# Optimization experiments

Hardware: AMD Instinct MI355X
Metric: run time of the kernel (lower is better)

Reference implementation:

```python
import jax, jax.numpy as jnp
import numpy as np
from jax import lax

L = 500
THRESH_INIT = 1.7
THRESH_STEP = 0.1
NUM_ADJ_PARM = 0.3


def _maxpool2(x):
    # 2x2 max pool, stride 2, NCHW
    return lax.reduce_window(x, -jnp.inf, lax.max, (1, 1, 2, 2), (1, 1, 2, 2), 'VALID')


def setup_inputs() -> dict:
    key = jax.random.key(0)
    ks = jax.random.split(key, 10)
    N = 2048
    s = 0.05
    return {
        'x': jax.random.normal(ks[0], (1, N, 1, 28, 28), dtype=jnp.float32),
        'conv1_w': jax.random.normal(ks[1], (20, 1, 5, 5), dtype=jnp.float32) * s,
        'conv1_b': jnp.zeros((20,), dtype=jnp.float32),
        'conv2_w': jax.random.normal(ks[2], (50, 20, 5, 5), dtype=jnp.float32) * s,
        'conv2_b': jnp.zeros((50,), dtype=jnp.float32),
        'fc_w': jax.random.normal(ks[3], (800, L), dtype=jnp.float32) * s,
        'fc_b': jnp.zeros((L,), dtype=jnp.float32),
        'gcn_w': jax.random.normal(ks[4], (L, L), dtype=jnp.float32) * s,
        'gcn_b': jnp.zeros((L,), dtype=jnp.float32),
    }


def reference(x, conv1_w, conv1_b, conv2_w, conv2_b, fc_w, fc_b, gcn_w, gcn_b):
    dn = ('NCHW', 'OIHW', 'NCHW')
    h = x[0]  # squeeze(0) -> [N,1,28,28]
    h = lax.conv_general_dilated(h, conv1_w, (1, 1), 'VALID', dimension_numbers=dn)
    h = _maxpool2(jax.nn.relu(h + conv1_b[None, :, None, None]))  # [N,20,12,12]
    h = lax.conv_general_dilated(h, conv2_w, (1, 1), 'VALID', dimension_numbers=dn)
    h = _maxpool2(jax.nn.relu(h + conv2_b[None, :, None, None]))  # [N,50,4,4]
    h = h.reshape(-1, 50 * 4 * 4)  # [N,800]
    H = jax.nn.relu(h @ fc_w + fc_b)  # [N,L]

    n_nodes = H.shape[0]
    sq = jnp.sum(H * H, axis=1)
    d2 = sq[:, None] + sq[None, :] - 2.0 * (H @ H.T)
    dist = jnp.sqrt(jnp.maximum(d2, 0.0))  # [N,N]

    eye = jnp.eye(n_nodes, dtype=bool)
    dist_sg = lax.stop_gradient(dist)
    min_edges = NUM_ADJ_PARM * n_nodes

    def cond(thr):
        cnt = jnp.sum(((dist_sg < thr) & ~eye).astype(jnp.float32))
        return cnt < min_edges

    thr = lax.while_loop(cond, lambda t: t + jnp.float32(THRESH_STEP),
                         jnp.float32(THRESH_INIT))

    adj = ((dist_sg < thr) & ~eye).astype(H.dtype)
    a_hat = adj + jnp.eye(n_nodes, dtype=H.dtype)
    dinv = lax.rsqrt(jnp.sum(a_hat, axis=1))  # deg >= 1 (self-loops)
    norm_adj = a_hat * dinv[:, None] * dinv[None, :]
    out = norm_adj @ (H @ gcn_w) + gcn_b  # [N,L]
    return jax.nn.log_softmax(out, axis=-1)
```

## Files before the change

### kernel.cpp

```cpp
#include <hip/hip_runtime.h>
#include <math.h>


#define NN 2048
#define LL 500
#define NBIN 512

#define KEEP(x) asm volatile("" : "+v"(x))

#define O_POOL1 ((size_t)0)
#define O_POOL2 (O_POOL1 + (size_t)2048*2880)
#define O_H     (O_POOL2 + (size_t)2048*800)
#define O_HW    (O_H     + (size_t)2048*500)
#define O_DIST  (O_HW    + (size_t)2048*500)
#define O_SQ    (O_DIST  + (size_t)2048*2048)
#define O_TBL   (O_SQ    + 2048)
#define O_HIST  (O_TBL   + NBIN)
#define O_THR   (O_HIST  + NBIN)
#define O_DINV  (O_THR   + 16)

__device__ __forceinline__ float4 ldg4_tail(const float* p, int rem) {
    float4 v;
    if (rem >= 4) v = *(const float4*)p;
    else {
        v.x = (rem > 0) ? p[0] : 0.f;
        v.y = (rem > 1) ? p[1] : 0.f;
        v.z = (rem > 2) ? p[2] : 0.f;
        v.w = (rem > 3) ? p[3] : 0.f;
    }
    return v;
}

__device__ __forceinline__ float4 zero4() { float4 v; v.x = v.y = v.z = v.w = 0.f; return v; }

__global__ void k_init(float* __restrict__ tbl, unsigned* __restrict__ hist) {
    int t = threadIdx.x;
    if (t == 0) {
        float v = 1.7f;
        for (int k = 0; k < NBIN; k++) { tbl[k] = v; v += 0.1f; }
    }
    for (int i = t; i < NBIN; i += 256) hist[i] = 0u;
}

__global__ __launch_bounds__(512)
void k_conv1(const float* __restrict__ x, const float* __restrict__ w,
             const float* __restrict__ b, float* __restrict__ out) {
    __shared__ float xin[4 * 784];
    int t = threadIdx.x;
    size_t n0 = (size_t)blockIdx.x * 4;
    {
        const float4* src = (const float4*)(x + n0 * 784);
        float4* dst = (float4*)xin;
        for (int i = t; i < 784; i += 512) dst[i] = src[i];
    }
    __syncthreads();
    for (int o = t; o < 576; o += 512) {
        int img = o / 144, p = o - img * 144, py = p / 12, px = p - py * 12;
        const float* xi = &xin[img * 784 + (2 * py) * 28 + 2 * px];
        float pt[36];
        #pragma unroll
        for (int r = 0; r < 6; r++)
            #pragma unroll
            for (int c = 0; c < 6; c++) { pt[r * 6 + c] = xi[r * 28 + c]; KEEP(pt[r * 6 + c]); }
        #pragma unroll
        for (int cb = 0; cb < 20; cb += 10) {
            float a0[10], a1[10], a2[10], a3[10];
            #pragma unroll
            for (int c = 0; c < 10; c++) { a0[c] = a1[c] = a2[c] = a3[c] = 0.f; }
            #pragma unroll
            for (int ky = 0; ky < 5; ky++)
                #pragma unroll
                for (int kx = 0; kx < 5; kx++) {
                    float p00 = pt[ky * 6 + kx],       p01 = pt[ky * 6 + kx + 1];
                    float p10 = pt[(ky + 1) * 6 + kx], p11 = pt[(ky + 1) * 6 + kx + 1];
                    #pragma unroll
                    for (int c = 0; c < 10; c++) {
                        float wv = w[(cb + c) * 25 + ky * 5 + kx];
                        a0[c] = fmaf(wv, p00, a0[c]); a1[c] = fmaf(wv, p01, a1[c]);
                        a2[c] = fmaf(wv, p10, a2[c]); a3[c] = fmaf(wv, p11, a3[c]);
                    }
                }
            #pragma unroll
            for (int c = 0; c < 10; c++) {
                float v = fmaxf(fmaxf(a0[c], a1[c]), fmaxf(a2[c], a3[c])) + b[cb + c];
                out[(n0 + img) * 2880 + (size_t)(cb + c) * 144 + p] = fmaxf(v, 0.f);
            }
        }
    }
}

__global__ __launch_bounds__(512)
void k_conv2(const float* __restrict__ in, const float* __restrict__ w,
             const float* __restrict__ b, float* __restrict__ out) {
    __shared__ float s_in[4 * 2888];
    int t = threadIdx.x;
    size_t n0 = (size_t)blockIdx.x * 4;
    for (int img = 0; img < 4; img++) {
        const float4* src = (const float4*)(in + (n0 + img) * 2880);
        float4* dst = (float4*)&s_in[img * 2888];
        for (int i = t; i < 720; i += 512) dst[i] = src[i];
    }
    __syncthreads();
    int lane = t & 63;
    int wv = __builtin_amdgcn_readfirstlane(t >> 6);
    int img = lane >> 4, p = lane & 15, py = p >> 2, px = p & 3;
    int cstart = wv * 7;
    const float* base = &s_in[img * 2888 + (2 * py) * 12 + 2 * px];
    float a0[7], a1[7], a2[7], a3[7];
    #pragma unroll
    for (int c = 0; c < 7; c++) { a0[c] = a1[c] = a2[c] = a3[c] = 0.f; }
    for (int ci = 0; ci < 20; ci++) {
        float pt[36];
        const float* bi = base + ci * 144;
        #pragma unroll
        for (int r = 0; r < 6; r++)
            #pragma unroll
            for (int c = 0; c < 6; c++) { pt[r * 6 + c] = bi[r * 12 + c]; KEEP(pt[r * 6 + c]); }
        #pragma unroll
        for (int ky = 0; ky < 5; ky++)
            #pragma unroll
            for (int kx = 0; kx < 5; kx++) {
                float p00 = pt[ky * 6 + kx],       p01 = pt[ky * 6 + kx + 1];
                float p10 = pt[(ky + 1) * 6 + kx], p11 = pt[(ky + 1) * 6 + kx + 1];
                #pragma unroll
                for (int cc = 0; cc < 7; cc++) {
                    int c = cstart + cc; int cm = (c < 50) ? c : 49;
                    float wt = w[cm * 500 + ci * 25 + ky * 5 + kx];
                    a0[cc] = fmaf(wt, p00, a0[cc]); a1[cc] = fmaf(wt, p01, a1[cc]);
                    a2[cc] = fmaf(wt, p10, a2[cc]); a3[cc] = fmaf(wt, p11, a3[cc]);
                }
            }
    }
    #pragma unroll
    for (int cc = 0; cc < 7; cc++) {
        int c = cstart + cc;
        if (c < 50) {
            float v = fmaxf(fmaxf(a0[cc], a1[cc]), fmaxf(a2[cc], a3[cc])) + b[c];
            out[(n0 + img) * 800 + c * 16 + p] = fmaxf(v, 0.f);
        }
    }
}

template <int RELU>
__global__ __launch_bounds__(256)
void k_gemm(const float* __restrict__ A, const float* __restrict__ B,
            float* __restrict__ C, int M, int N, int K,
            const float* __restrict__ bias) {
    __shared__ __align__(16) float As[32][68];
    __shared__ __align__(16) float Bs[32][36];
    int t = threadIdx.x;
    int m0 = blockIdx.y * 64, n0 = blockIdx.x * 32;
    int ar = t >> 3, ac = (t & 7) * 4;
    int br = t >> 3, bc = (t & 7) * 4;
    int ty = t >> 4, tx = t & 15;
    float acc[4][2] = {};
    float4 pa0, pa1, pb0;

#define GM_LOAD(k0) do {                                                       \
        int remk = K - ((k0) + ac);                                            \
        pa0 = ldg4_tail(&A[(size_t)(m0 + ar) * K + (k0) + ac], remk);          \
        pa1 = ldg4_tail(&A[(size_t)(m0 + ar + 32) * K + (k0) + ac], remk);     \
        pb0 = ((k0) + br < K)                                                  \
            ? ldg4_tail(&B[(size_t)((k0) + br) * N + n0 + bc], N - (n0 + bc))  \
            : zero4();                                                         \
    } while (0)

#define GM_STORE() do {                                                       \
        As[ac + 0][ar] = pa0.x; As[ac + 1][ar] = pa0.y;                        \
        As[ac + 2][ar] = pa0.z; As[ac + 3][ar] = pa0.w;                        \
        As[ac + 0][ar + 32] = pa1.x; As[ac + 1][ar + 32] = pa1.y;              \
        As[ac + 2][ar + 32] = pa1.z; As[ac + 3][ar + 32] = pa1.w;              \
        *(float4*)&Bs[br][bc] = pb0;                                           \
    } while (0)

    GM_LOAD(0); GM_STORE(); __syncthreads();
    for (int k0 = 0; k0 < K; k0 += 32) {
        bool more = (k0 + 32) < K;
        if (more) GM_LOAD(k0 + 32);
        #pragma unroll
        for (int kk = 0; kk < 32; kk++) {
            float4 a4 = *(const float4*)&As[kk][ty * 4];
            float2 b2 = *(const float2*)&Bs[kk][tx * 2];
            float av[4] = {a4.x, a4.y, a4.z, a4.w};
            float bv[2] = {b2.x, b2.y};
            #pragma unroll
            for (int i = 0; i < 4; i++)
                #pragma unroll
                for (int j = 0; j < 2; j++) acc[i][j] = fmaf(av[i], bv[j], acc[i][j]);
        }
        __syncthreads();
        if (more) { GM_STORE(); __syncthreads(); }
    }
#undef GM_LOAD
#undef GM_STORE

    #pragma unroll
    for (int i = 0; i < 4; i++) {
        int row = m0 + ty * 4 + i;
        int c0 = n0 + tx * 2;
        #pragma unroll
        for (int j = 0; j < 2; j++) {
            if (c0 + j < N) {
                float a = acc[i][j];
                if (RELU) { a += bias[c0 + j]; a = fmaxf(a, 0.f); }
                C[(size_t)row * N + c0 + j] = a;
            }
        }
    }
}

__global__ __launch_bounds__(256)
void k_rowsq(const float* __restrict__ H, float* __restrict__ sq) {
    int t = threadIdx.x, lane = t & 63, wv = t >> 6;
    int row = blockIdx.x * 4 + wv;
    const float* h = &H[(size_t)row * LL];
    float s = 0.f;
    for (int j = lane; j < LL; j += 64) { float v = h[j]; s = fmaf(v, v, s); }
    #pragma unroll
    for (int o = 32; o > 0; o >>= 1) s += __shfl_down(s, o, 64);
    if (lane == 0) sq[row] = s;
}

__global__ __launch_bounds__(256)
void k_dist(const float* __restrict__ Hm, float* __restrict__ C,
            const float* __restrict__ sq, const float* __restrict__ tbl_g,
            unsigned* __restrict__ hist_g) {
    __shared__ __align__(16) float As[32][132];
    __shared__ __align__(16) float Bs[32][68];
    __shared__ float tbl_s[NBIN];
    __shared__ unsigned hist_s[NBIN];
    const int K = LL, N = NN;
    int t = threadIdx.x;
    int m0 = blockIdx.y * 128, n0 = blockIdx.x * 64;
    for (int i = t; i < NBIN; i += 256) { tbl_s[i] = tbl_g[i]; hist_s[i] = 0u; }
    float acc[8][4] = {};
    int alr = t >> 3, alc = (t & 7) * 4;
    int bnr = t >> 2, bkc = (t & 3) * 4;
    int ty = t >> 4, tx = t & 15;
    float4 pa0, pa1, pa2, pa3, pb0, pb1;

#define DIST_LOAD(k0) do {                                                     \
        int rem = K - ((k0) + alc);                                            \
        pa0 = ldg4_tail(&Hm[(size_t)(m0 + alr) * K + (k0) + alc], rem);        \
        pa1 = ldg4_tail(&Hm[(size_t)(m0 + alr + 32) * K + (k0) + alc], rem);   \
        pa2 = ldg4_tail(&Hm[(size_t)(m0 + alr + 64) * K + (k0) + alc], rem);   \
        pa3 = ldg4_tail(&Hm[(size_t)(m0 + alr + 96) * K + (k0) + alc], rem);   \
        int rb0 = K - ((k0) + bkc); int rb1 = K - ((k0) + bkc + 16);           \
        pb0 = ldg4_tail(&Hm[(size_t)(n0 + bnr) * K + (k0) + bkc], rb0);        \
        pb1 = ldg4_tail(&Hm[(size_t)(n0 + bnr) * K + (k0) + bkc + 16], rb1);   \
    } while (0)

#define DIST_STORE() do {                                                      \
        As[alc + 0][alr] = pa0.x; As[alc + 1][alr] = pa0.y;                    \
        As[alc + 2][alr] = pa0.z; As[alc + 3][alr] = pa0.w;                    \
        As[alc + 0][alr + 32] = pa1.x; As[alc + 1][alr + 32] = pa1.y;          \
        As[alc + 2][alr + 32] = pa1.z; As[alc + 3][alr + 32] = pa1.w;          \
        As[alc + 0][alr + 64] = pa2.x; As[alc + 1][alr + 64] = pa2.y;          \
        As[alc + 2][alr + 64] = pa2.z; As[alc + 3][alr + 64] = pa2.w;          \
        As[alc + 0][alr + 96] = pa3.x; As[alc + 1][alr + 96] = pa3.y;          \
        As[alc + 2][alr + 96] = pa3.z; As[alc + 3][alr + 96] = pa3.w;          \
        Bs[bkc + 0][bnr] = pb0.x; Bs[bkc + 1][bnr] = pb0.y;                    \
        Bs[bkc + 2][bnr] = pb0.z; Bs[bkc + 3][bnr] = pb0.w;                    \
        Bs[bkc + 16][bnr] = pb1.x; Bs[bkc + 17][bnr] = pb1.y;                  \
        Bs[bkc + 18][bnr] = pb1.z; Bs[bkc + 19][bnr] = pb1.w;                  \
    } while (0)

    DIST_LOAD(0); DIST_STORE(); __syncthreads();
    for (int k0 = 0; k0 < K; k0 += 32) {
        bool more = (k0 + 32) < K;
        if (more) DIST_LOAD(k0 + 32);
        #pragma unroll
        for (int kk = 0; kk < 32; kk++) {
            float4 A0 = *(const float4*)&As[kk][ty * 8];
            float4 A1 = *(const float4*)&As[kk][ty * 8 + 4];
            float4 B0 = *(const float4*)&Bs[kk][tx * 4];
            float av[8] = {A0.x, A0.y, A0.z, A0.w, A1.x, A1.y, A1.z, A1.w};
            float bv[4] = {B0.x, B0.y, B0.z, B0.w};
            #pragma unroll
            for (int i = 0; i < 8; i++)
                #pragma unroll
                for (int j = 0; j < 4; j++) acc[i][j] = fmaf(av[i], bv[j], acc[i][j]);
        }
        __syncthreads();
        if (more) { DIST_STORE(); __syncthreads(); }
    }
#undef DIST_LOAD
#undef DIST_STORE

    float4 sqj = *(const float4*)&sq[n0 + tx * 4];
    float sqjv[4] = {sqj.x, sqj.y, sqj.z, sqj.w};
    #pragma unroll
    for (int ii = 0; ii < 8; ii++) {
        int i = m0 + ty * 8 + ii;
        float sqi = sq[i];
        int c0 = n0 + tx * 4;
        float dd[4];
        #pragma unroll
        for (int j = 0; j < 4; j++) {
            int col = c0 + j;
            float d2 = sqi + sqjv[j] - 2.0f * acc[ii][j];
            float d = sqrtf(fmaxf(d2, 0.f));
            dd[j] = d;
            if (col != i) {
                int bb = (int)ceilf((d - 1.7f) * 10.0f);
                bb = bb < 0 ? 0 : (bb > NBIN - 1 ? NBIN - 1 : bb);
                while (bb > 0 && d < tbl_s[bb - 1]) --bb;
                while (bb < NBIN - 1 && d >= tbl_s[bb]) ++bb;
                if (d < tbl_s[bb]) atomicAdd(&hist_s[bb], 1u);
            }
        }
        float4 dv; dv.x = dd[0]; dv.y = dd[1]; dv.z = dd[2]; dv.w = dd[3];
        *(float4*)&C[(size_t)i * N + c0] = dv;
    }
    __syncthreads();
    for (int idx = t; idx < NBIN; idx += 256)
        if (hist_s[idx]) atomicAdd(&hist_g[idx], hist_s[idx]);
}

__global__ __launch_bounds__(256)
void k_pick(const unsigned* __restrict__ hist, const float* __restrict__ tbl,
            float* __restrict__ thrbuf) {
    __shared__ unsigned ps[256];
    __shared__ int sel;
    int t = threadIdx.x;
    if (t == 0) sel = NBIN - 1;
    unsigned v0 = hist[2 * t], v1 = hist[2 * t + 1];
    unsigned s = v0 + v1;
    ps[t] = s;
    __syncthreads();
    for (int o = 1; o < 256; o <<= 1) {
        unsigned add = (t >= o) ? ps[t - o] : 0u;
        __syncthreads();
        ps[t] += add;
        __syncthreads();
    }
    unsigned c = ps[t] - s;
    int f = -1;
    c += v0; if (c >= 615u) f = 2 * t;
    else { c += v1; if (c >= 615u) f = 2 * t + 1; }
    if (f >= 0) atomicMin(&sel, f);
    __syncthreads();
    if (t == 0) thrbuf[0] = tbl[sel];
}

__global__ __launch_bounds__(256)
void k_deg(const float* __restrict__ dist, const float* __restrict__ thrbuf,
           float* __restrict__ dinv) {
    int t = threadIdx.x, lane = t & 63, wv = t >> 6;
    int row = blockIdx.x * 4 + wv;
    float thr = thrbuf[0];
    const float4* dr4 = (const float4*)&dist[(size_t)row * NN];
    int cnt = 0;
    #pragma unroll
    for (int bq = 0; bq < 8; bq++) {
        int i4 = bq * 64 + lane;
        float4 v = dr4[i4];
        int j = i4 * 4;
        cnt += (v.x < thr && j + 0 != row) ? 1 : 0;
        cnt += (v.y < thr && j + 1 != row) ? 1 : 0;
        cnt += (v.z < thr && j + 2 != row) ? 1 : 0;
        cnt += (v.w < thr && j + 3 != row) ? 1 : 0;
    }
    #pragma unroll
    for (int o = 32; o > 0; o >>= 1) cnt += __shfl_down(cnt, o, 64);
    if (lane == 0) dinv[row] = 1.0f / sqrtf((float)(cnt + 1));
}

__global__ __launch_bounds__(256)
void k_gcn(const float* __restrict__ dist, const float* __restrict__ thrbuf,
           const float* __restrict__ dinv, const float* __restrict__ HW,
           const float* __restrict__ bias, float* __restrict__ outp) {
    __shared__ int nbr[2048];
    __shared__ float ndv[2048];
    __shared__ unsigned cnts[256];
    __shared__ float red[16];
    int t = threadIdx.x, lane = t & 63, wv = t >> 6;
    int i = blockIdx.x;
    float thr = thrbuf[0];
    const float* dr = &dist[(size_t)i * NN];
    float4 q0 = *(const float4*)&dr[t * 8];
    float4 q1 = *(const float4*)&dr[t * 8 + 4];
    float dv[8] = {q0.x, q0.y, q0.z, q0.w, q1.x, q1.y, q1.z, q1.w};
    unsigned lc = 0;
    #pragma unroll
    for (int q = 0; q < 8; q++) lc += (dv[q] < thr && (t * 8 + q) != i) ? 1u : 0u;
    cnts[t] = lc;
    __syncthreads();
    for (int o = 1; o < 256; o <<= 1) {
        unsigned add = (t >= o) ? cnts[t - o] : 0u;
        __syncthreads();
        cnts[t] += add;
        __syncthreads();
    }
    unsigned pos = cnts[t] - lc;
    int nn = (int)cnts[255];
    #pragma unroll
    for (int q = 0; q < 8; q++) {
        int j = t * 8 + q;
        if (dv[q] < thr && j != i) { nbr[pos] = j; ndv[pos] = dinv[j]; pos++; }
    }
    __syncthreads();
    float di = dinv[i];
    float v0, v1 = -1e30f, mx;
    {
        int d = t;
        float s = di * HW[(size_t)i * LL + d];
        for (int m = 0; m < nn; m++) s += ndv[m] * HW[(size_t)nbr[m] * LL + d];
        v0 = di * s + bias[d];
        mx = v0;
    }
    if (t + 256 < LL) {
        int d = t + 256;
        float s = di * HW[(size_t)i * LL + d];
        for (int m = 0; m < nn; m++) s += ndv[m] * HW[(size_t)nbr[m] * LL + d];
        v1 = di * s + bias[d];
        mx = fmaxf(mx, v1);
    }
    #pragma unroll
    for (int o = 32; o > 0; o >>= 1) mx = fmaxf(mx, __shfl_down(mx, o, 64));
    if (lane == 0) red[wv] = mx;
    __syncthreads();
    mx = fmaxf(fmaxf(red[0], red[1]), fmaxf(red[2], red[3]));
    float es = expf(v0 - mx) + ((t + 256 < LL) ? expf(v1 - mx) : 0.f);
    #pragma unroll
    for (int o = 32; o > 0; o >>= 1) es += __shfl_down(es, o, 64);
    if (lane == 0) red[8 + wv] = es;
    __syncthreads();
    float lse = logf(red[8] + red[9] + red[10] + red[11]);
    outp[(size_t)i * LL + t] = v0 - mx - lse;
    if (t + 256 < LL) outp[(size_t)i * LL + t + 256] = v1 - mx - lse;
}

extern "C" void kernel_launch(void* const* d_in, const int* in_sizes, int n_in,
                              void* d_out, int out_size, void* d_ws, size_t ws_size,
                              hipStream_t stream) {
    (void)in_sizes; (void)n_in; (void)out_size; (void)ws_size;
    const float* x   = (const float*)d_in[0];
    const float* c1w = (const float*)d_in[1];
    const float* c1b = (const float*)d_in[2];
    const float* c2w = (const float*)d_in[3];
    const float* c2b = (const float*)d_in[4];
    const float* fcw = (const float*)d_in[5];
    const float* fcb = (const float*)d_in[6];
    const float* gw  = (const float*)d_in[7];
    const float* gb  = (const float*)d_in[8];

    float* ws = (float*)d_ws;
    float* pool1 = ws + O_POOL1;
    float* pool2 = ws + O_POOL2;
    float* H     = ws + O_H;
    float* HWp   = ws + O_HW;
    float* distm = ws + O_DIST;
    float* sqv   = ws + O_SQ;
    float* tbl   = ws + O_TBL;
    unsigned* hist = (unsigned*)(ws + O_HIST);
    float* thr   = ws + O_THR;
    float* dinv  = ws + O_DINV;

    k_init<<<1, 256, 0, stream>>>(tbl, hist);
    k_conv1<<<512, 512, 0, stream>>>(x, c1w, c1b, pool1);
    k_conv2<<<512, 512, 0, stream>>>(pool1, c2w, c2b, pool2);
    k_gemm<1><<<dim3(16, 32), 256, 0, stream>>>(pool2, fcw, H, 2048, 500, 800, fcb);
    k_rowsq<<<512, 256, 0, stream>>>(H, sqv);
    k_dist<<<dim3(32, 16), 256, 0, stream>>>(H, distm, sqv, tbl, hist);
    k_pick<<<1, 256, 0, stream>>>(hist, tbl, thr);
    k_deg<<<512, 256, 0, stream>>>(distm, thr, dinv);
    k_gemm<0><<<dim3(16, 32), 256, 0, stream>>>(H, gw, HWp, 2048, 500, 500, nullptr);
    k_gcn<<<2048, 256, 0, stream>>>(distm, thr, dinv, HWp, gb, (float*)d_out);
}
```

Measured before the change: 370.7 us.

## Split-K larger-tile GEMMs, wider dist tiles, padded conv LDS, 10-wave conv2

Replaces the small-tile 64x32 GEMM with a 128x128 split-K GEMM that writes four partial sums into the reused pool1 buffer, then reduces them in a separate fuse kernel that also applies bias and ReLU. The H@gcn_w GEMM is moved earlier and uses the same path. The distance kernel tile grows from 128x64 to 128x128 for more reuse per block, at the cost of fewer blocks. The conv kernels pad shared-memory rows to reduce bank conflicts, and conv2 runs 640 threads so that 10 waves each handle 5 channels with no clamped wasted channels. The split-K path adds extra partial-sum traffic and two extra launches.

```diff
diff --git a/kernel.cpp b/kernel.cpp
--- a/kernel.cpp
+++ b/kernel.cpp
@@ -18,6 +18,7 @@
 #define O_HIST  (O_TBL   + NBIN)
 #define O_THR   (O_HIST  + NBIN)
 #define O_DINV  (O_THR   + 16)
+#define PSZ     ((size_t)2048 * 500)
 
 __device__ __forceinline__ float4 ldg4_tail(const float* p, int rem) {
     float4 v;
@@ -30,7 +31,6 @@
     }
     return v;
 }
-
 __device__ __forceinline__ float4 zero4() { float4 v; v.x = v.y = v.z = v.w = 0.f; return v; }
 
 __global__ void k_init(float* __restrict__ tbl, unsigned* __restrict__ hist) {
@@ -45,18 +45,19 @@
 __global__ __launch_bounds__(512)
 void k_conv1(const float* __restrict__ x, const float* __restrict__ w,
              const float* __restrict__ b, float* __restrict__ out) {
-    __shared__ float xin[4 * 784];
+    __shared__ float xin[4 * 785];
     int t = threadIdx.x;
     size_t n0 = (size_t)blockIdx.x * 4;
-    {
-        const float4* src = (const float4*)(x + n0 * 784);
-        float4* dst = (float4*)xin;
-        for (int i = t; i < 784; i += 512) dst[i] = src[i];
+    for (int i = t; i < 784; i += 512) {
+        float4 v = ((const float4*)(x + n0 * 784))[i];
+        int img = i / 196, off = (i - img * 196) * 4;
+        float* d = &xin[img * 785 + off];
+        d[0] = v.x; d[1] = v.y; d[2] = v.z; d[3] = v.w;
     }
     __syncthreads();
     for (int o = t; o < 576; o += 512) {
         int img = o / 144, p = o - img * 144, py = p / 12, px = p - py * 12;
-        const float* xi = &xin[img * 784 + (2 * py) * 28 + 2 * px];
+        const float* xi = &xin[img * 785 + (2 * py) * 28 + 2 * px];
         float pt[36];
         #pragma unroll
         for (int r = 0; r < 6; r++)
@@ -89,26 +90,30 @@
     }
 }
 
-__global__ __launch_bounds__(512)
+__global__ __launch_bounds__(640)
 void k_conv2(const float* __restrict__ in, const float* __restrict__ w,
              const float* __restrict__ b, float* __restrict__ out) {
-    __shared__ float s_in[4 * 2888];
+    __shared__ float s_in[4 * 2881];
     int t = threadIdx.x;
     size_t n0 = (size_t)blockIdx.x * 4;
     for (int img = 0; img < 4; img++) {
         const float4* src = (const float4*)(in + (n0 + img) * 2880);
-        float4* dst = (float4*)&s_in[img * 2888];
-        for (int i = t; i < 720; i += 512) dst[i] = src[i];
+        float* dst = &s_in[img * 2881];
+        for (int i = t; i < 720; i += 640) {
+            float4 v = src[i];
+            float* d = dst + i * 4;
+            d[0] = v.x; d[1] = v.y; d[2] = v.z; d[3] = v.w;
+        }
     }
     __syncthreads();
     int lane = t & 63;
     int wv = __builtin_amdgcn_readfirstlane(t >> 6);
     int img = lane >> 4, p = lane & 15, py = p >> 2, px = p & 3;
-    int cstart = wv * 7;
-    const float* base = &s_in[img * 2888 + (2 * py) * 12 + 2 * px];
-    float a0[7], a1[7], a2[7], a3[7];
-    #pragma unroll
-    for (int c = 0; c < 7; c++) { a0[c] = a1[c] = a2[c] = a3[c] = 0.f; }
+    int cstart = wv * 5;
+    const float* base = &s_in[img * 2881 + (2 * py) * 12 + 2 * px];
+    float a0[5], a1[5], a2[5], a3[5];
+    #pragma unroll
+    for (int c = 0; c < 5; c++) { a0[c] = a1[c] = a2[c] = a3[c] = 0.f; }
     for (int ci = 0; ci < 20; ci++) {
         float pt[36];
         const float* bi = base + ci * 144;
@@ -123,90 +128,137 @@
                 float p00 = pt[ky * 6 + kx],       p01 = pt[ky * 6 + kx + 1];
                 float p10 = pt[(ky + 1) * 6 + kx], p11 = pt[(ky + 1) * 6 + kx + 1];
                 #pragma unroll
-                for (int cc = 0; cc < 7; cc++) {
-                    int c = cstart + cc; int cm = (c < 50) ? c : 49;
-                    float wt = w[cm * 500 + ci * 25 + ky * 5 + kx];
+                for (int cc = 0; cc < 5; cc++) {
+                    float wt = w[(cstart + cc) * 500 + ci * 25 + ky * 5 + kx];
                     a0[cc] = fmaf(wt, p00, a0[cc]); a1[cc] = fmaf(wt, p01, a1[cc]);
                     a2[cc] = fmaf(wt, p10, a2[cc]); a3[cc] = fmaf(wt, p11, a3[cc]);
                 }
             }
     }
     #pragma unroll
-    for (int cc = 0; cc < 7; cc++) {
+    for (int cc = 0; cc < 5; cc++) {
         int c = cstart + cc;
-        if (c < 50) {
-            float v = fmaxf(fmaxf(a0[cc], a1[cc]), fmaxf(a2[cc], a3[cc])) + b[c];
-            out[(n0 + img) * 800 + c * 16 + p] = fmaxf(v, 0.f);
-        }
-    }
-}
-
-template <int RELU>
-__global__ __launch_bounds__(256)
-void k_gemm(const float* __restrict__ A, const float* __restrict__ B,
-            float* __restrict__ C, int M, int N, int K,
-            const float* __restrict__ bias) {
-    __shared__ __align__(16) float As[32][68];
-    __shared__ __align__(16) float Bs[32][36];
+        float v = fmaxf(fmaxf(a0[cc], a1[cc]), fmaxf(a2[cc], a3[cc])) + b[c];
+        out[(n0 + img) * 800 + c * 16 + p] = fmaxf(v, 0.f);
+    }
+}
+
+__global__ __launch_bounds__(256)
+void k_gemmsp(const float* __restrict__ A, const float* __restrict__ B,
+              float* __restrict__ Cpart, int M, int N, int K, int kchunk) {
+    __shared__ __align__(16) float As[32][132];
+    __shared__ __align__(16) float Bs[32][132];
     int t = threadIdx.x;
-    int m0 = blockIdx.y * 64, n0 = blockIdx.x * 32;
-    int ar = t >> 3, ac = (t & 7) * 4;
-    int br = t >> 3, bc = (t & 7) * 4;
+    int m0 = blockIdx.y * 128, n0 = blockIdx.x * 128;
+    int part = blockIdx.z;
+    int kbeg = part * kchunk;
+    int kend = kbeg + kchunk; if (kend > K) kend = K;
+    float* Cp = Cpart + (size_t)part * M * N;
+
+    int ar = t >> 3, akc = (t & 7) * 4;
+    int bkr = t >> 4, bc = (t & 15) * 4;
     int ty = t >> 4, tx = t & 15;
-    float acc[4][2] = {};
-    float4 pa0, pa1, pb0;
-
-#define GM_LOAD(k0) do {                                                       \
-        int remk = K - ((k0) + ac);                                            \
-        pa0 = ldg4_tail(&A[(size_t)(m0 + ar) * K + (k0) + ac], remk);          \
-        pa1 = ldg4_tail(&A[(size_t)(m0 + ar + 32) * K + (k0) + ac], remk);     \
-        pb0 = ((k0) + br < K)                                                  \
-            ? ldg4_tail(&B[(size_t)((k0) + br) * N + n0 + bc], N - (n0 + bc))  \
-            : zero4();                                                         \
+    float acc[8][8] = {};
+    float4 pa[4], pb[4];
+
+#define SP_LOAD(k0) do {                                                        \
+        int rem = kend - ((k0) + akc);                                          \
+        pa[0] = ldg4_tail(&A[(size_t)(m0 + ar)      * K + (k0) + akc], rem);    \
+        pa[1] = ldg4_tail(&A[(size_t)(m0 + ar + 32) * K + (k0) + akc], rem);    \
+        pa[2] = ldg4_tail(&A[(size_t)(m0 + ar + 64) * K + (k0) + akc], rem);    \
+        pa[3] = ldg4_tail(&A[(size_t)(m0 + ar + 96) * K + (k0) + akc], rem);    \
+        int rn0 = N - (n0 + bc), rn1 = N - (n0 + bc + 64);                      \
+        pb[0] = ((k0) + bkr < kend)                                             \
+              ? ldg4_tail(&B[(size_t)((k0) + bkr) * N + n0 + bc], rn0) : zero4(); \
+        pb[1] = ((k0) + bkr < kend)                                             \
+              ? ldg4_tail(&B[(size_t)((k0) + bkr) * N + n0 + bc + 64], rn1) : zero4(); \
+        pb[2] = ((k0) + bkr + 16 < kend)                                        \
+              ? ldg4_tail(&B[(size_t)((k0) + bkr + 16) * N + n0 + bc], rn0) : zero4(); \
+        pb[3] = ((k0) + bkr + 16 < kend)                                        \
+              ? ldg4_tail(&B[(size_t)((k0) + bkr + 16) * N + n0 + bc + 64], rn1) : zero4(); \
     } while (0)
 
-#define GM_STORE() do {                                                       \
-        As[ac + 0][ar] = pa0.x; As[ac + 1][ar] = pa0.y;                        \
-        As[ac + 2][ar] = pa0.z; As[ac + 3][ar] = pa0.w;                        \
-        As[ac + 0][ar + 32] = pa1.x; As[ac + 1][ar + 32] = pa1.y;              \
-        As[ac + 2][ar + 32] = pa1.z; As[ac + 3][ar + 32] = pa1.w;              \
-        *(float4*)&Bs[br][bc] = pb0;                                           \
+#define SP_STORE() do {                                                         \
+        for (int g = 0; g < 4; g++) {                                           \
+            As[akc + 0][ar + 32 * g] = pa[g].x; As[akc + 1][ar + 32 * g] = pa[g].y; \
+            As[akc + 2][ar + 32 * g] = pa[g].z; As[akc + 3][ar + 32 * g] = pa[g].w; \
+        }                                                                       \
+        *(float4*)&Bs[bkr][bc]           = pb[0];                               \
+        *(float4*)&Bs[bkr][bc + 64]      = pb[1];                               \
+        *(float4*)&Bs[bkr + 16][bc]      = pb[2];                               \
+        *(float4*)&Bs[bkr + 16][bc + 64] = pb[3];                               \
     } while (0)
 
-    GM_LOAD(0); GM_STORE(); __syncthreads();
-    for (int k0 = 0; k0 < K; k0 += 32) {
-        bool more = (k0 + 32) < K;
-        if (more) GM_LOAD(k0 + 32);
+    SP_LOAD(kbeg); SP_STORE(); __syncthreads();
+    for (int k0 = kbeg; k0 < kend; k0 += 32) {
+        bool more = (k0 + 32) < kend;
+        if (more) SP_LOAD(k0 + 32);
         #pragma unroll
         for (int kk = 0; kk < 32; kk++) {
-            float4 a4 = *(const float4*)&As[kk][ty * 4];
-            float2 b2 = *(const float2*)&Bs[kk][tx * 2];
-            float av[4] = {a4.x, a4.y, a4.z, a4.w};
-            float bv[2] = {b2.x, b2.y};
-            #pragma unroll
-            for (int i = 0; i < 4; i++)
+            float4 A0 = *(const float4*)&As[kk][ty * 8];
+            float4 A1 = *(const float4*)&As[kk][ty * 8 + 4];
+            float4 B0 = *(const float4*)&Bs[kk][tx * 4];
+            float4 B1 = *(const float4*)&Bs[kk][64 + tx * 4];
+            float av[8] = {A0.x, A0.y, A0.z, A0.w, A1.x, A1.y, A1.z, A1.w};
+            float bv[8] = {B0.x, B0.y, B0.z, B0.w, B1.x, B1.y, B1.z, B1.w};
+            #pragma unroll
+            for (int i = 0; i < 8; i++)
                 #pragma unroll
-                for (int j = 0; j < 2; j++) acc[i][j] = fmaf(av[i], bv[j], acc[i][j]);
+                for (int j = 0; j < 8; j++) acc[i][j] = fmaf(av[i], bv[j], acc[i][j]);
         }
         __syncthreads();
-        if (more) { GM_STORE(); __syncthreads(); }
-    }
-#undef GM_LOAD
-#undef GM_STORE
-
-    #pragma unroll
-    for (int i = 0; i < 4; i++) {
-        int row = m0 + ty * 4 + i;
-        int c0 = n0 + tx * 2;
-        #pragma unroll
-        for (int j = 0; j < 2; j++) {
-            if (c0 + j < N) {
-                float a = acc[i][j];
-                if (RELU) { a += bias[c0 + j]; a = fmaxf(a, 0.f); }
-                C[(size_t)row * N + c0 + j] = a;
+        if (more) { SP_STORE(); __syncthreads(); }
+    }
+#undef SP_LOAD
+#undef SP_STORE
+
+    #pragma unroll
+    for (int ii = 0; ii < 8; ii++) {
+        int row = m0 + ty * 8 + ii;
+        #pragma unroll
+        for (int g = 0; g < 2; g++) {
+            int c0 = n0 + g * 64 + tx * 4;
+            if (c0 + 3 < N) {
+                float4 vv;
+                vv.x = acc[ii][g * 4 + 0]; vv.y = acc[ii][g * 4 + 1];
+                vv.z = acc[ii][g * 4 + 2]; vv.w = acc[ii][g * 4 + 3];
+                *(float4*)&Cp[(size_t)row * N + c0] = vv;
+            } else {
+                #pragma unroll
+                for (int j = 0; j < 4; j++)
+                    if (c0 + j < N) Cp[(size_t)row * N + c0 + j] = acc[ii][g * 4 + j];
             }
         }
     }
+}
+
+__global__ __launch_bounds__(256)
+void k_fuse(const float* __restrict__ parts, float* __restrict__ out,
+            const float* __restrict__ bias, int relu) {
+    int i4 = blockIdx.x * 256 + threadIdx.x;
+    size_t off = (size_t)i4 * 4;
+    float4 s = *(const float4*)&parts[off];
+    #pragma unroll
+    for (int p = 1; p < 4; p++) {
+        float4 v = *(const float4*)&parts[p * PSZ + off];
+        s.x += v.x; s.y += v.y; s.z += v.z; s.w += v.w;
+    }
+    float vv[4] = {s.x, s.y, s.z, s.w};
+    if (bias) {
+        int base = i4 * 4;
+        int col0 = base - (base / LL) * LL;
+        #pragma unroll
+        for (int j = 0; j < 4; j++) {
+            int c = col0 + j; if (c >= LL) c -= LL;
+            vv[j] += bias[c];
+        }
+    }
+    if (relu) {
+        #pragma unroll
+        for (int j = 0; j < 4; j++) vv[j] = fmaxf(vv[j], 0.f);
+    }
+    float4 o; o.x = vv[0]; o.y = vv[1]; o.z = vv[2]; o.w = vv[3];
+    *(float4*)&out[off] = o;
 }
 
 __global__ __launch_bounds__(256)
@@ -226,91 +278,89 @@
             const float* __restrict__ sq, const float* __restrict__ tbl_g,
             unsigned* __restrict__ hist_g) {
     __shared__ __align__(16) float As[32][132];
-    __shared__ __align__(16) float Bs[32][68];
+    __shared__ __align__(16) float Bs[32][132];
     __shared__ float tbl_s[NBIN];
     __shared__ unsigned hist_s[NBIN];
     const int K = LL, N = NN;
     int t = threadIdx.x;
-    int m0 = blockIdx.y * 128, n0 = blockIdx.x * 64;
+    int m0 = blockIdx.y * 128, n0 = blockIdx.x * 128;
     for (int i = t; i < NBIN; i += 256) { tbl_s[i] = tbl_g[i]; hist_s[i] = 0u; }
-    float acc[8][4] = {};
-    int alr = t >> 3, alc = (t & 7) * 4;
-    int bnr = t >> 2, bkc = (t & 3) * 4;
+    float acc[8][8] = {};
+    int lr = t >> 3, lkc = (t & 7) * 4;
     int ty = t >> 4, tx = t & 15;
-    float4 pa0, pa1, pa2, pa3, pb0, pb1;
-
-#define DIST_LOAD(k0) do {                                                     \
-        int rem = K - ((k0) + alc);                                            \
-        pa0 = ldg4_tail(&Hm[(size_t)(m0 + alr) * K + (k0) + alc], rem);        \
-        pa1 = ldg4_tail(&Hm[(size_t)(m0 + alr + 32) * K + (k0) + alc], rem);   \
-        pa2 = ldg4_tail(&Hm[(size_t)(m0 + alr + 64) * K + (k0) + alc], rem);   \
-        pa3 = ldg4_tail(&Hm[(size_t)(m0 + alr + 96) * K + (k0) + alc], rem);   \
-        int rb0 = K - ((k0) + bkc); int rb1 = K - ((k0) + bkc + 16);           \
-        pb0 = ldg4_tail(&Hm[(size_t)(n0 + bnr) * K + (k0) + bkc], rb0);        \
-        pb1 = ldg4_tail(&Hm[(size_t)(n0 + bnr) * K + (k0) + bkc + 16], rb1);   \
+    float4 pa[4], pb[4];
+
+#define D_LOAD(k0) do {                                                         \
+        int rem = K - ((k0) + lkc);                                             \
+        pa[0] = ldg4_tail(&Hm[(size_t)(m0 + lr)      * K + (k0) + lkc], rem);   \
+        pa[1] = ldg4_tail(&Hm[(size_t)(m0 + lr + 32) * K + (k0) + lkc], rem);   \
+        pa[2] = ldg4_tail(&Hm[(size_t)(m0 + lr + 64) * K + (k0) + lkc], rem);   \
+        pa[3] = ldg4_tail(&Hm[(size_t)(m0 + lr + 96) * K + (k0) + lkc], rem);   \
+        pb[0] = ldg4_tail(&Hm[(size_t)(n0 + lr)      * K + (k0) + lkc], rem);   \
+        pb[1] = ldg4_tail(&Hm[(size_t)(n0 + lr + 32) * K + (k0) + lkc], rem);   \
+        pb[2] = ldg4_tail(&Hm[(size_t)(n0 + lr + 64) * K + (k0) + lkc], rem);   \
+        pb[3] = ldg4_tail(&Hm[(size_t)(n0 + lr + 96) * K + (k0) + lkc], rem);   \
     } while (0)
 
-#define DIST_STORE() do {                                                      \
-        As[alc + 0][alr] = pa0.x; As[alc + 1][alr] = pa0.y;                    \
-        As[alc + 2][alr] = pa0.z; As[alc + 3][alr] = pa0.w;                    \
-        As[alc + 0][alr + 32] = pa1.x; As[alc + 1][alr + 32] = pa1.y;          \
-        As[alc + 2][alr + 32] = pa1.z; As[alc + 3][alr + 32] = pa1.w;          \
-        As[alc + 0][alr + 64] = pa2.x; As[alc + 1][alr + 64] = pa2.y;          \
-        As[alc + 2][alr + 64] = pa2.z; As[alc + 3][alr + 64] = pa2.w;          \
-        As[alc + 0][alr + 96] = pa3.x; As[alc + 1][alr + 96] = pa3.y;          \
-        As[alc + 2][alr + 96] = pa3.z; As[alc + 3][alr + 96] = pa3.w;          \
-        Bs[bkc + 0][bnr] = pb0.x; Bs[bkc + 1][bnr] = pb0.y;                    \
-        Bs[bkc + 2][bnr] = pb0.z; Bs[bkc + 3][bnr] = pb0.w;                    \
-        Bs[bkc + 16][bnr] = pb1.x; Bs[bkc + 17][bnr] = pb1.y;                  \
-        Bs[bkc + 18][bnr] = pb1.z; Bs[bkc + 19][bnr] = pb1.w;                  \
+#define D_STORE() do {                                                          \
+        for (int g = 0; g < 4; g++) {                                           \
+            As[lkc + 0][lr + 32 * g] = pa[g].x; As[lkc + 1][lr + 32 * g] = pa[g].y; \
+            As[lkc + 2][lr + 32 * g] = pa[g].z; As[lkc + 3][lr + 32 * g] = pa[g].w; \
+            Bs[lkc + 0][lr + 32 * g] = pb[g].x; Bs[lkc + 1][lr + 32 * g] = pb[g].y; \
+            Bs[lkc + 2][lr + 32 * g] = pb[g].z; Bs[lkc + 3][lr + 32 * g] = pb[g].w; \
+        }                                                                       \
     } while (0)
 
-    DIST_LOAD(0); DIST_STORE(); __syncthreads();
+    D_LOAD(0); D_STORE(); __syncthreads();
     for (int k0 = 0; k0 < K; k0 += 32) {
         bool more = (k0 + 32) < K;
-        if (more) DIST_LOAD(k0 + 32);
+        if (more) D_LOAD(k0 + 32);
         #pragma unroll
         for (int kk = 0; kk < 32; kk++) {
             float4 A0 = *(const float4*)&As[kk][ty * 8];
             float4 A1 = *(const float4*)&As[kk][ty * 8 + 4];
             float4 B0 = *(const float4*)&Bs[kk][tx * 4];
+            float4 B1 = *(const float4*)&Bs[kk][64 + tx * 4];
             float av[8] = {A0.x, A0.y, A0.z, A0.w, A1.x, A1.y, A1.z, A1.w};
-            float bv[4] = {B0.x, B0.y, B0.z, B0.w};
+            float bv[8] = {B0.x, B0.y, B0.z, B0.w, B1.x, B1.y, B1.z, B1.w};
             #pragma unroll
             for (int i = 0; i < 8; i++)
                 #pragma unroll
-                for (int j = 0; j < 4; j++) acc[i][j] = fmaf(av[i], bv[j], acc[i][j]);
+                for (int j = 0; j < 8; j++) acc[i][j] = fmaf(av[i], bv[j], acc[i][j]);
         }
         __syncthreads();
-        if (more) { DIST_STORE(); __syncthreads(); }
-    }
-#undef DIST_LOAD
-#undef DIST_STORE
-
-    float4 sqj = *(const float4*)&sq[n0 + tx * 4];
-    float sqjv[4] = {sqj.x, sqj.y, sqj.z, sqj.w};
+        if (more) { D_STORE(); __syncthreads(); }
+    }
+#undef D_LOAD
+#undef D_STORE
+
     #pragma unroll
     for (int ii = 0; ii < 8; ii++) {
         int i = m0 + ty * 8 + ii;
         float sqi = sq[i];
-        int c0 = n0 + tx * 4;
-        float dd[4];
-        #pragma unroll
-        for (int j = 0; j < 4; j++) {
-            int col = c0 + j;
-            float d2 = sqi + sqjv[j] - 2.0f * acc[ii][j];
-            float d = sqrtf(fmaxf(d2, 0.f));
-            dd[j] = d;
-            if (col != i) {
-                int bb = (int)ceilf((d - 1.7f) * 10.0f);
-                bb = bb < 0 ? 0 : (bb > NBIN - 1 ? NBIN - 1 : bb);
-                while (bb > 0 && d < tbl_s[bb - 1]) --bb;
-                while (bb < NBIN - 1 && d >= tbl_s[bb]) ++bb;
-                if (d < tbl_s[bb]) atomicAdd(&hist_s[bb], 1u);
+        #pragma unroll
+        for (int g = 0; g < 2; g++) {
+            int c0 = n0 + g * 64 + tx * 4;
+            float4 sqj = *(const float4*)&sq[c0];
+            float sqjv[4] = {sqj.x, sqj.y, sqj.z, sqj.w};
+            float dd[4];
+            #pragma unroll
+            for (int j = 0; j < 4; j++) {
+                int col = c0 + j;
+                float d2 = sqi + sqjv[j] - 2.0f * acc[ii][g * 4 + j];
+                float d = sqrtf(fmaxf(d2, 0.f));
+                dd[j] = d;
+                if (col != i) {
+                    int bb = (int)ceilf((d - 1.7f) * 10.0f);
+                    bb = bb < 0 ? 0 : (bb > NBIN - 1 ? NBIN - 1 : bb);
+                    while (bb > 0 && d < tbl_s[bb - 1]) --bb;
+                    while (bb < NBIN - 1 && d >= tbl_s[bb]) ++bb;
+                    if (d < tbl_s[bb]) atomicAdd(&hist_s[bb], 1u);
+                }
             }
-        }
-        float4 dv; dv.x = dd[0]; dv.y = dd[1]; dv.z = dd[2]; dv.w = dd[3];
-        *(float4*)&C[(size_t)i * N + c0] = dv;
+            float4 dv; dv.x = dd[0]; dv.y = dd[1]; dv.z = dd[2]; dv.w = dd[3];
+            *(float4*)&C[(size_t)i * N + c0] = dv;
+        }
     }
     __syncthreads();
     for (int idx = t; idx < NBIN; idx += 256)
@@ -456,15 +506,18 @@
     unsigned* hist = (unsigned*)(ws + O_HIST);
     float* thr   = ws + O_THR;
     float* dinv  = ws + O_DINV;
+    float* part  = pool1;
 
     k_init<<<1, 256, 0, stream>>>(tbl, hist);
     k_conv1<<<512, 512, 0, stream>>>(x, c1w, c1b, pool1);
-    k_conv2<<<512, 512, 0, stream>>>(pool1, c2w, c2b, pool2);
-    k_gemm<1><<<dim3(16, 32), 256, 0, stream>>>(pool2, fcw, H, 2048, 500, 800, fcb);
+    k_conv2<<<512, 640, 0, stream>>>(pool1, c2w, c2b, pool2);
+    k_gemmsp<<<dim3(4, 16, 4), 256, 0, stream>>>(pool2, fcw, part, 2048, 500, 800, 200);
+    k_fuse<<<1000, 256, 0, stream>>>(part, H, fcb, 1);
+    k_gemmsp<<<dim3(4, 16, 4), 256, 0, stream>>>(H, gw, part, 2048, 500, 500, 128);
+    k_fuse<<<1000, 256, 0, stream>>>(part, HWp, nullptr, 0);
     k_rowsq<<<512, 256, 0, stream>>>(H, sqv);
-    k_dist<<<dim3(32, 16), 256, 0, stream>>>(H, distm, sqv, tbl, hist);
+    k_dist<<<dim3(16, 16), 256, 0, stream>>>(H, distm, sqv, tbl, hist);
     k_pick<<<1, 256, 0, stream>>>(hist, tbl, thr);
     k_deg<<<512, 256, 0, stream>>>(distm, thr, dinv);
-    k_gemm<0><<<dim3(16, 32), 256, 0, stream>>>(H, gw, HWp, 2048, 500, 500, nullptr);
     k_gcn<<<2048, 256, 0, stream>>>(distm, thr, dinv, HWp, gb, (float*)d_out);
 }
```

Measured after the change: 493.7 us. 33.2% more time.
